# Kernel tuning notes

Measured on AMD Instinct MI355X. Metric: run time of the kernel, lower is better.

The kernel has to match this reference:

```python
import jax, jax.numpy as jnp
import numpy as np

B, N, M = 64, 1024, 4096
HID, OUT = 2048, 512

def setup_inputs() -> dict:
    key = jax.random.key(0)
    ks = jax.random.split(key, 10)
    s = 0.02  # weight init scale
    return {
        "pos": jax.random.normal(ks[0], (B, N, 3), dtype=jnp.float32),
        "basis": jax.random.normal(ks[1], (M, 3), dtype=jnp.float32),
        "W0": jax.random.normal(ks[2], (N, HID), dtype=jnp.float32) * s,
        "b0": jnp.zeros((HID,), dtype=jnp.float32),
        "W1": jax.random.normal(ks[3], (HID, HID), dtype=jnp.float32) * s,
        "b1": jnp.zeros((HID,), dtype=jnp.float32),
        "W2": jax.random.normal(ks[4], (HID, HID), dtype=jnp.float32) * s,
        "b2": jnp.zeros((HID,), dtype=jnp.float32),
        "W3": jax.random.normal(ks[5], (HID, OUT), dtype=jnp.float32) * s,
        "b3": jnp.zeros((OUT,), dtype=jnp.float32),
    }

def reference(pos, basis, W0, b0, W1, b1, W2, b2, W3, b3):
    # pairwise Euclidean distances: [B, N, M] via ||p||^2 + ||q||^2 - 2 p.q
    p2 = jnp.sum(pos * pos, axis=-1, keepdims=True)            # [B, N, 1]
    q2 = jnp.sum(basis * basis, axis=-1)                       # [M]
    pq = jnp.einsum('bnc,mc->bnm', pos, basis)                 # [B, N, M]
    d2 = p2 + q2[None, None, :] - 2.0 * pq
    dists = jnp.sqrt(jnp.maximum(d2, 1e-12))                   # [B, N, M]
    x = jnp.min(dists, axis=2)                                 # [B, N] -> MLP in_dim = N
    # MLP (eval mode: dropout identity, norm=None, plain last layer)
    x = jax.nn.relu(x @ W0 + b0)
    x = jax.nn.relu(x @ W1 + b1)
    x = jax.nn.relu(x @ W2 + b2)
    return x @ W3 + b3                                         # [B, OUT]
```

## Files before the change

### kernel.cpp

```cpp
#include <hip/hip_runtime.h>
#include <hip/hip_bf16.h>
#include <math.h>

#define B_SZ   64
#define N_SZ   1024
#define M_SZ   4096
#define HID_SZ 2048
#define OUT_SZ 512

#define AS1 __attribute__((address_space(1)))
#define AS3 __attribute__((address_space(3)))

__global__ __launch_bounds__(256, 2) void dist_min_kernel(
    const float* __restrict__ pos,
    const float* __restrict__ basis,
    float* __restrict__ xT)
{
  const int tid  = threadIdx.x;
  const int lane = tid & 63;
  const int wave = tid >> 6;

  float nqx[16], nqy[16], nqz[16], qc[16];
#pragma unroll
  for (int i = 0; i < 16; ++i) {
    int j = wave * 1024 + i * 64 + lane;
    float qx = basis[3*j+0], qy = basis[3*j+1], qz = basis[3*j+2];
    nqx[i] = -qx; nqy[i] = -qy; nqz[i] = -qz;
    qc[i]  = 0.5f * (qx*qx + qy*qy + qz*qz);
  }

  __shared__ float red[16][256];
  const int pbase = blockIdx.x * 128;

  for (int c = 0; c < 8; ++c) {
    const int cbase = pbase + c * 16;
    const float* pp = pos + (size_t)3 * cbase;
    float pc[48];
#pragma unroll
    for (int e = 0; e < 48; ++e) pc[e] = pp[e];

#pragma unroll
    for (int p = 0; p < 16; ++p) {
      const float px = pc[3*p+0], py = pc[3*p+1], pz = pc[3*p+2];
      float t[16];
#pragma unroll
      for (int i = 0; i < 16; ++i) t[i] = fmaf(nqx[i], px, qc[i]);
#pragma unroll
      for (int i = 0; i < 16; ++i) t[i] = fmaf(nqy[i], py, t[i]);
#pragma unroll
      for (int i = 0; i < 16; ++i) t[i] = fmaf(nqz[i], pz, t[i]);
      float m0 = fminf(fminf(t[0],  t[1]),  t[2]);
      float m1 = fminf(fminf(t[3],  t[4]),  t[5]);
      float m2 = fminf(fminf(t[6],  t[7]),  t[8]);
      float m3 = fminf(fminf(t[9],  t[10]), t[11]);
      float m4 = fminf(fminf(t[12], t[13]), t[14]);
      float r0 = fminf(fminf(m0, m1), m2);
      float r1 = fminf(fminf(m3, m4), t[15]);
      red[p][tid] = fminf(r0, r1);
    }
    __syncthreads();

    {
      const int p   = tid >> 4;
      const int sub = tid & 15;
      const float4* r4 = (const float4*)&red[p][sub * 16];
      float4 v0 = r4[0], v1 = r4[1], v2 = r4[2], v3 = r4[3];
      float w0 = fminf(fminf(v0.x, v0.y), fminf(v0.z, v0.w));
      float w1 = fminf(fminf(v1.x, v1.y), fminf(v1.z, v1.w));
      float w2 = fminf(fminf(v2.x, v2.y), fminf(v2.z, v2.w));
      float w3 = fminf(fminf(v3.x, v3.y), fminf(v3.z, v3.w));
      float v  = fminf(fminf(w0, w1), fminf(w2, w3));
#pragma unroll
      for (int o = 1; o < 16; o <<= 1) v = fminf(v, __shfl_xor(v, o));
      if (sub == 0) {
        int i = cbase + p;
        float px = pos[3*i+0], py = pos[3*i+1], pz = pos[3*i+2];
        float p2 = px*px + py*py + pz*pz;
        float d2 = fmaf(2.f, v, p2);
        d2 = fmaxf(d2, 1e-12f);
        int n = i & (N_SZ - 1);
        int b = i >> 10;
        xT[n * 64 + b] = sqrtf(d2);
      }
    }
    __syncthreads();
  }
}

template <int K, int J, int JT, int KSPAN>
__global__ __launch_bounds__(256, 2) void gemm4_kernel(
    const float* __restrict__ xT,
    const float* __restrict__ W,
    float* __restrict__ P)
{
  constexpr int WCHUNK = 64;
  constexpr int NSTEP  = KSPAN / WCHUNK;
  const int jt   = blockIdx.x % JT;
  const int s    = blockIdx.x / JT;
  const int tid  = threadIdx.x;
  const int lane = tid & 63;
  const int wave = tid >> 6;
  const int jl = lane & 15;
  const int bq = lane >> 4;
  const int j0 = jt * 64 + jl * 4;
  const int b0 = wave * 16 + bq * 4;

  __shared__ __align__(16) float xs[KSPAN][64];
  __shared__ __align__(16) float wring[2][WCHUNK][64];

  {
    const float4* sx = (const float4*)(xT + (size_t)s * KSPAN * 64);
    float4* dx = (float4*)&xs[0][0];
#pragma unroll
    for (int i = 0; i < KSPAN / 16; ++i)
      dx[i * 256 + tid] = sx[i * 256 + tid];
  }

  const float* wbase = W + ((size_t)s * KSPAN + wave * 16 + (lane >> 4)) * J
                         + jt * 64 + (lane & 15) * 4;

#pragma unroll
  for (int d = 0; d < 4; ++d)
    __builtin_amdgcn_global_load_lds(
        (const AS1 void*)(wbase + (size_t)(d * 4) * J),
        (AS3 void*)&wring[0][wave * 16 + d * 4][0], 16, 0, 0);
  asm volatile("s_waitcnt vmcnt(0)" ::: "memory");
  __syncthreads();

  float acc[4][4];
#pragma unroll
  for (int a = 0; a < 4; ++a)
#pragma unroll
    for (int c = 0; c < 4; ++c) acc[a][c] = 0.f;

#pragma unroll 1
  for (int t = 0; t < NSTEP; ++t) {
    const int buf = t & 1;
    if (t + 1 < NSTEP) {
#pragma unroll
      for (int d = 0; d < 4; ++d)
        __builtin_amdgcn_global_load_lds(
            (const AS1 void*)(wbase + (size_t)((t + 1) * WCHUNK + d * 4) * J),
            (AS3 void*)&wring[buf ^ 1][wave * 16 + d * 4][0], 16, 0, 0);
    }
#pragma unroll 8
    for (int r = 0; r < WCHUNK; ++r) {
      float4 w4 = *(const float4*)&wring[buf][r][jl * 4];
      float4 x4 = *(const float4*)&xs[t * WCHUNK + r][b0];
      const float wv[4] = {w4.x, w4.y, w4.z, w4.w};
      const float xv[4] = {x4.x, x4.y, x4.z, x4.w};
#pragma unroll
      for (int a = 0; a < 4; ++a)
#pragma unroll
        for (int c = 0; c < 4; ++c)
          acc[a][c] = fmaf(xv[a], wv[c], acc[a][c]);
    }
    if (t + 1 < NSTEP) {
      asm volatile("s_waitcnt vmcnt(0)" ::: "memory");
      __syncthreads();
    }
  }

#pragma unroll
  for (int c = 0; c < 4; ++c) {
    float4 o = make_float4(acc[0][c], acc[1][c], acc[2][c], acc[3][c]);
    *(float4*)(P + ((size_t)s * J + (j0 + c)) * 64 + b0) = o;
  }
}

template <int J, int KS, bool RELU, bool TRANS>
__global__ __launch_bounds__(256) void reduce_bias_kernel(
    const float* __restrict__ P,
    const float* __restrict__ bias,
    float* __restrict__ out)
{
  const int t = blockIdx.x * 256 + threadIdx.x;
  const int b = t & 63;
  const int j = t >> 6;
  float v = 0.f;
#pragma unroll
  for (int s = 0; s < KS; ++s) v += P[((size_t)s * J + j) * 64 + b];
  v += bias[j];
  if (RELU) v = fmaxf(v, 0.f);
  if (TRANS) out[j * 64 + b] = v;
  else       out[(size_t)b * J + j] = v;
}

extern "C" void kernel_launch(void* const* d_in, const int* in_sizes, int n_in,
                              void* d_out, int out_size, void* d_ws, size_t ws_size,
                              hipStream_t stream) {
  const float* pos   = (const float*)d_in[0];
  const float* basis = (const float*)d_in[1];
  const float* W0    = (const float*)d_in[2];
  const float* b0    = (const float*)d_in[3];
  const float* W1    = (const float*)d_in[4];
  const float* b1    = (const float*)d_in[5];
  const float* W2    = (const float*)d_in[6];
  const float* b2    = (const float*)d_in[7];
  const float* W3    = (const float*)d_in[8];
  const float* b3    = (const float*)d_in[9];
  float* out = (float*)d_out;

  char* ws = (char*)d_ws;
  float* P  = (float*)ws;
  float* xA = (float*)(ws + (8u << 20));
  float* xB = (float*)(ws + (8u << 20) + (512u << 10));

  dist_min_kernel<<<512, 256, 0, stream>>>(pos, basis, xA);

  gemm4_kernel<1024, HID_SZ, 32, 128>
      <<<8 * 32, 256, 0, stream>>>(xA, W0, P);
  reduce_bias_kernel<HID_SZ, 8, true, true>
      <<<HID_SZ * 64 / 256, 256, 0, stream>>>(P, b0, xB);

  gemm4_kernel<2048, HID_SZ, 32, 128>
      <<<16 * 32, 256, 0, stream>>>(xB, W1, P);
  reduce_bias_kernel<HID_SZ, 16, true, true>
      <<<HID_SZ * 64 / 256, 256, 0, stream>>>(P, b1, xA);

  gemm4_kernel<2048, HID_SZ, 32, 128>
      <<<16 * 32, 256, 0, stream>>>(xA, W2, P);
  reduce_bias_kernel<HID_SZ, 16, true, true>
      <<<HID_SZ * 64 / 256, 256, 0, stream>>>(P, b2, xB);

  gemm4_kernel<2048, OUT_SZ, 8, 64>
      <<<32 * 8, 256, 0, stream>>>(xB, W3, P);
  reduce_bias_kernel<OUT_SZ, 32, false, false>
      <<<OUT_SZ * 64 / 256, 256, 0, stream>>>(P, b3, out);
}
```

Measured before the change: 178.9 us.

## Stream GEMM weights straight to registers with double-buffered prefetch instead of LDS

The split-K GEMM kernels no longer stage weight tiles through a double-buffered LDS ring filled by global_load_lds. Each thread now loads its own float4 weight columns straight from global memory into two register sets, prefetching the next 8 rows while computing on the current 8. This drops the LDS weight staging and the per-chunk barriers. The cost is more registers, and the four waves of a block each load the same weight rows independently, relying on cache to absorb the repeats.

```diff
diff --git a/kernel.cpp b/kernel.cpp
--- a/kernel.cpp
+++ b/kernel.cpp
@@ -7,9 +7,6 @@
 #define M_SZ   4096
 #define HID_SZ 2048
 #define OUT_SZ 512
-
-#define AS1 __attribute__((address_space(1)))
-#define AS3 __attribute__((address_space(3)))
 
 __global__ __launch_bounds__(256, 2) void dist_min_kernel(
     const float* __restrict__ pos,
@@ -88,13 +85,11 @@
 }
 
 template <int K, int J, int JT, int KSPAN>
-__global__ __launch_bounds__(256, 2) void gemm4_kernel(
+__global__ __launch_bounds__(256, 2) void gemm6_kernel(
     const float* __restrict__ xT,
     const float* __restrict__ W,
     float* __restrict__ P)
 {
-  constexpr int WCHUNK = 64;
-  constexpr int NSTEP  = KSPAN / WCHUNK;
   const int jt   = blockIdx.x % JT;
   const int s    = blockIdx.x / JT;
   const int tid  = threadIdx.x;
@@ -106,7 +101,6 @@
   const int b0 = wave * 16 + bq * 4;
 
   __shared__ __align__(16) float xs[KSPAN][64];
-  __shared__ __align__(16) float wring[2][WCHUNK][64];
 
   {
     const float4* sx = (const float4*)(xT + (size_t)s * KSPAN * 64);
@@ -115,39 +109,31 @@
     for (int i = 0; i < KSPAN / 16; ++i)
       dx[i * 256 + tid] = sx[i * 256 + tid];
   }
-
-  const float* wbase = W + ((size_t)s * KSPAN + wave * 16 + (lane >> 4)) * J
-                         + jt * 64 + (lane & 15) * 4;
-
-#pragma unroll
-  for (int d = 0; d < 4; ++d)
-    __builtin_amdgcn_global_load_lds(
-        (const AS1 void*)(wbase + (size_t)(d * 4) * J),
-        (AS3 void*)&wring[0][wave * 16 + d * 4][0], 16, 0, 0);
-  asm volatile("s_waitcnt vmcnt(0)" ::: "memory");
   __syncthreads();
 
+  const float* wq = W + (size_t)s * KSPAN * J + j0;
+
   float acc[4][4];
 #pragma unroll
   for (int a = 0; a < 4; ++a)
 #pragma unroll
     for (int c = 0; c < 4; ++c) acc[a][c] = 0.f;
 
+  float4 A[8], Bf[8];
+
+#pragma unroll
+  for (int u = 0; u < 8; ++u)
+    A[u] = *(const float4*)(wq + (size_t)u * J);
+
 #pragma unroll 1
-  for (int t = 0; t < NSTEP; ++t) {
-    const int buf = t & 1;
-    if (t + 1 < NSTEP) {
-#pragma unroll
-      for (int d = 0; d < 4; ++d)
-        __builtin_amdgcn_global_load_lds(
-            (const AS1 void*)(wbase + (size_t)((t + 1) * WCHUNK + d * 4) * J),
-            (AS3 void*)&wring[buf ^ 1][wave * 16 + d * 4][0], 16, 0, 0);
-    }
-#pragma unroll 8
-    for (int r = 0; r < WCHUNK; ++r) {
-      float4 w4 = *(const float4*)&wring[buf][r][jl * 4];
-      float4 x4 = *(const float4*)&xs[t * WCHUNK + r][b0];
-      const float wv[4] = {w4.x, w4.y, w4.z, w4.w};
+  for (int kk = 0; kk < KSPAN; kk += 16) {
+#pragma unroll
+    for (int u = 0; u < 8; ++u)
+      Bf[u] = *(const float4*)(wq + (size_t)(kk + 8 + u) * J);
+#pragma unroll
+    for (int u = 0; u < 8; ++u) {
+      float4 x4 = *(const float4*)&xs[kk + u][b0];
+      const float wv[4] = {A[u].x, A[u].y, A[u].z, A[u].w};
       const float xv[4] = {x4.x, x4.y, x4.z, x4.w};
 #pragma unroll
       for (int a = 0; a < 4; ++a)
@@ -155,9 +141,21 @@
         for (int c = 0; c < 4; ++c)
           acc[a][c] = fmaf(xv[a], wv[c], acc[a][c]);
     }
-    if (t + 1 < NSTEP) {
-      asm volatile("s_waitcnt vmcnt(0)" ::: "memory");
-      __syncthreads();
+    if (kk + 16 < KSPAN) {
+#pragma unroll
+      for (int u = 0; u < 8; ++u)
+        A[u] = *(const float4*)(wq + (size_t)(kk + 16 + u) * J);
+    }
+#pragma unroll
+    for (int u = 0; u < 8; ++u) {
+      float4 x4 = *(const float4*)&xs[kk + 8 + u][b0];
+      const float wv[4] = {Bf[u].x, Bf[u].y, Bf[u].z, Bf[u].w};
+      const float xv[4] = {x4.x, x4.y, x4.z, x4.w};
+#pragma unroll
+      for (int a = 0; a < 4; ++a)
+#pragma unroll
+        for (int c = 0; c < 4; ++c)
+          acc[a][c] = fmaf(xv[a], wv[c], acc[a][c]);
     }
   }
 
@@ -170,8 +168,7 @@
 
 template <int J, int KS, bool RELU, bool TRANS>
 __global__ __launch_bounds__(256) void reduce_bias_kernel(
-    const float* __restrict__ P,
-    const float* __restrict__ bias,
+    const float* __restrict__ P, const float* __restrict__ bias,
     float* __restrict__ out)
 {
   const int t = blockIdx.x * 256 + threadIdx.x;
@@ -208,23 +205,19 @@
 
   dist_min_kernel<<<512, 256, 0, stream>>>(pos, basis, xA);
 
-  gemm4_kernel<1024, HID_SZ, 32, 128>
-      <<<8 * 32, 256, 0, stream>>>(xA, W0, P);
+  gemm6_kernel<1024, HID_SZ, 32, 128><<<8 * 32, 256, 0, stream>>>(xA, W0, P);
   reduce_bias_kernel<HID_SZ, 8, true, true>
       <<<HID_SZ * 64 / 256, 256, 0, stream>>>(P, b0, xB);
 
-  gemm4_kernel<2048, HID_SZ, 32, 128>
-      <<<16 * 32, 256, 0, stream>>>(xB, W1, P);
+  gemm6_kernel<2048, HID_SZ, 32, 128><<<16 * 32, 256, 0, stream>>>(xB, W1, P);
   reduce_bias_kernel<HID_SZ, 16, true, true>
       <<<HID_SZ * 64 / 256, 256, 0, stream>>>(P, b1, xA);
 
-  gemm4_kernel<2048, HID_SZ, 32, 128>
-      <<<16 * 32, 256, 0, stream>>>(xA, W2, P);
+  gemm6_kernel<2048, HID_SZ, 32, 128><<<16 * 32, 256, 0, stream>>>(xA, W2, P);
   reduce_bias_kernel<HID_SZ, 16, true, true>
       <<<HID_SZ * 64 / 256, 256, 0, stream>>>(P, b2, xB);
 
-  gemm4_kernel<2048, OUT_SZ, 8, 64>
-      <<<32 * 8, 256, 0, stream>>>(xB, W3, P);
+  gemm6_kernel<2048, OUT_SZ, 8, 64><<<32 * 8, 256, 0, stream>>>(xB, W3, P);
   reduce_bias_kernel<OUT_SZ, 32, false, false>
       <<<OUT_SZ * 64 / 256, 256, 0, stream>>>(P, b3, out);
 }
```

New measurement: 182.8 us. 1.02x slower.
